# Kernel tuning notes

Measured on AMD Instinct MI355X. Metric: run time of the kernel, lower is better.

## Reference

```python
import jax, jax.numpy as jnp
import numpy as np

N_NODES = 50000
N_EDGES = 800000
D_IN = 64
D_HID = 64
D_OUT = 16


def setup_inputs() -> dict:
    key = jax.random.key(0)
    ks = jax.random.split(key, 20)
    features = jax.random.normal(ks[0], (N_NODES, D_IN), dtype=jnp.float32)
    src = jax.random.randint(ks[1], (N_EDGES,), 0, N_NODES)
    dst = jax.random.randint(ks[2], (N_EDGES,), 0, N_NODES)

    def lin(k, din, dout):
        bound = 1.0 / np.sqrt(din)
        k1, k2 = jax.random.split(k)
        W = jax.random.uniform(k1, (din, dout), jnp.float32, -bound, bound)
        b = jax.random.uniform(k2, (dout,), jnp.float32, -bound, bound)
        return W, b

    W0a, b0a = lin(ks[3], D_IN, D_HID)
    W0b, b0b = lin(ks[4], D_HID, D_HID)
    W1a, b1a = lin(ks[5], D_HID, D_HID)
    W1b, b1b = lin(ks[6], D_HID, D_HID)
    W2a, b2a = lin(ks[7], D_HID, D_HID)
    W2b, b2b = lin(ks[8], D_HID, D_HID)
    Wout, bout = lin(ks[9], D_HID, D_OUT)
    return {
        "features": features, "src": src, "dst": dst,
        "W0a": W0a, "b0a": b0a, "W0b": W0b, "b0b": b0b,
        "W1a": W1a, "b1a": b1a, "W1b": W1b, "b1b": b1b,
        "W2a": W2a, "b2a": b2a, "W2b": W2b, "b2b": b2b,
        "Wout": Wout, "bout": bout,
    }


def reference(features, src, dst,
              W0a, b0a, W0b, b0b,
              W1a, b1a, W1b, b1b,
              W2a, b2a, W2b, b2b,
              Wout, bout):
    N = features.shape[0]

    def gin_layer(h, Wa, ba, Wb, bb):
        # GINConv 'sum': gather source features along edges, scatter-sum to dst
        agg = jax.ops.segment_sum(h[src], dst, num_segments=N)  # [N, D]
        r = h + agg  # (1 + eps) * h + agg with eps = 0 (DGL default)
        # ApplyNodeFunc MLP: Linear -> ReLU -> Linear
        return jax.nn.relu(r @ Wa + ba) @ Wb + bb

    h = gin_layer(features, W0a, b0a, W0b, b0b)
    h = gin_layer(h, W1a, b1a, W1b, b1b)
    h = gin_layer(h, W2a, b2a, W2b, b2b)
    # dgl.mean_nodes over the single graph -> [1, D_HID]
    hg = jnp.mean(h, axis=0, keepdims=True)
    return hg @ Wout + bout  # [1, D_OUT]
```

## Files before the change

### kernel.cpp

```cpp
#include <hip/hip_runtime.h>
#include <hip/hip_bf16.h>


#define NNODES 50000
#define NEDGES 800000
#define DDIM   64
#define DOUT   16

#define CHUNK  4096
#define NB1    196
#define NBUCK  196
#define NB64   782
#define CVTB   1024

#define KCAP   1408

typedef unsigned int uint;
typedef unsigned short ushort;
typedef __attribute__((ext_vector_type(8))) short bf16x8;
typedef __attribute__((ext_vector_type(4))) float f32x4;
typedef __attribute__((ext_vector_type(2))) float f32x2;

#define LSTR 72

static __device__ __forceinline__ uint f2bf(float f) {
    uint u = __float_as_uint(f);
    return (u + 0x7fffu + ((u >> 16) & 1u)) >> 16;
}
static __device__ __forceinline__ float bf_lo(uint u) { return __uint_as_float(u << 16); }
static __device__ __forceinline__ float bf_hi(uint u) { return __uint_as_float(u & 0xffff0000u); }

#define ACC4(vv) do { f32x2 u_;                                   \
    u_.x = bf_lo((vv).x); u_.y = bf_hi((vv).x); c0 += u_;         \
    u_.x = bf_lo((vv).y); u_.y = bf_hi((vv).y); c1 += u_;         \
    u_.x = bf_lo((vv).z); u_.y = bf_hi((vv).z); c2 += u_;         \
    u_.x = bf_lo((vv).w); u_.y = bf_hi((vv).w); c3 += u_; } while (0)


__global__ __launch_bounds__(256) void s1_kernel(const int* __restrict__ src,
                                                 const int* __restrict__ dst,
                                                 uint* __restrict__ key,
                                                 int* __restrict__ gh,
                                                 const float2* __restrict__ fin,
                                                 uint* __restrict__ hb0,
                                                 uint* __restrict__ hb1,
                                                 const float* __restrict__ Wa0,
                                                 const float* __restrict__ Wb0,
                                                 const float* __restrict__ Wa1,
                                                 const float* __restrict__ Wb1,
                                                 const float* __restrict__ Wa2,
                                                 const float* __restrict__ Wb2,
                                                 uint* __restrict__ wWT,
                                                 float* __restrict__ part,
                                                 int* __restrict__ ticket) {
    __shared__ int h[NBUCK];
    int blk = blockIdx.x;
    int t = threadIdx.x;
    if (blk < NB1) {
        for (int i = t; i < NBUCK; i += 256) h[i] = 0;
        __syncthreads();
        int base = blk * CHUNK;
        int end = base + CHUNK < NEDGES ? base + CHUNK : NEDGES;
        for (int i = base + t; i < end; i += 256) {
            int d = dst[i];
            key[i] = ((uint)d << 16) | (uint)src[i];
            atomicAdd(&h[d >> 8], 1);
        }
        __syncthreads();
        for (int i = t; i < NBUCK; i += 256) gh[blk * NBUCK + i] = h[i];
        return;
    }
    int m = blk - NB1;
    if (m < CVTB) {
        for (int i = m * 256 + t; i < (NNODES + 1) * 32; i += CVTB * 256) {
            uint r = 0u;
            if (i < NNODES * 32) {
                float2 v = fin[i];
                r = f2bf(v.x) | (f2bf(v.y) << 16);
            }
            hb0[i] = r;
        }
        return;
    }
    m -= CVTB;
    if (m < 6) {
        const float* Wm = (m == 0) ? Wa0 : (m == 1) ? Wb0 : (m == 2) ? Wa1
                        : (m == 3) ? Wb1 : (m == 4) ? Wa2 : Wb2;
        for (int o = t; o < 2048; o += 256) {
            int nn = o >> 5, kk = o & 31;
            wWT[m * 2048 + o] = f2bf(Wm[(2 * kk) * 64 + nn]) |
                                (f2bf(Wm[(2 * kk + 1) * 64 + nn]) << 16);
        }
        return;
    }
    if (t < 64) part[t] = 0.f;
    if (t == 64) *ticket = 0;
    if (t >= 128 && t < 160) hb1[NNODES * 32 + (t - 128)] = 0u;
}


__global__ __launch_bounds__(256) void sort_offsets_a_kernel(const int* __restrict__ gh,
                                                             int* __restrict__ offraw,
                                                             int* __restrict__ tot) {
    __shared__ int s[256];
    int b = blockIdx.x;
    int i = threadIdx.x;
    int v = (i < NB1) ? gh[i * NBUCK + b] : 0;
    s[i] = v;
    __syncthreads();
    for (int off = 1; off < 256; off <<= 1) {
        int add = (i >= off) ? s[i - off] : 0;
        __syncthreads();
        s[i] += add;
        __syncthreads();
    }
    if (i < NB1) offraw[i * NBUCK + b] = s[i] - v;
    if (i == 255) tot[b] = s[255];
}


__global__ __launch_bounds__(256) void sort_scatter1_kernel(const uint* __restrict__ key,
                                                            const int* __restrict__ offraw,
                                                            const int* __restrict__ tot,
                                                            uint* __restrict__ out) {
    __shared__ int s[256];
    __shared__ int cur[NBUCK];
    int blk = blockIdx.x;
    int t = threadIdx.x;
    int v = (t < NBUCK) ? tot[t] : 0;
    s[t] = v;
    __syncthreads();
    for (int off = 1; off < 256; off <<= 1) {
        int add = (t >= off) ? s[t - off] : 0;
        __syncthreads();
        s[t] += add;
        __syncthreads();
    }
    if (t < NBUCK) cur[t] = (s[t] - v) + offraw[blk * NBUCK + t];
    __syncthreads();
    int base = blk * CHUNK;
    int end = base + CHUNK < NEDGES ? base + CHUNK : NEDGES;
    for (int j = base + t; j < end; j += 256) {
        uint k = key[j];
        int pos = atomicAdd(&cur[k >> 24], 1);
        out[pos] = k;
    }
}


__global__ __launch_bounds__(256) void sort_bucket_kernel(const uint* __restrict__ in,
                                                          const int* __restrict__ tot,
                                                          int* __restrict__ rowptr,
                                                          uint* __restrict__ out) {
    __shared__ int s[256];
    __shared__ int hh[256];
    __shared__ int cur[256];
    __shared__ int slo[2];
    int blk = blockIdx.x;
    int t = threadIdx.x;
    int v = (t < NBUCK) ? tot[t] : 0;
    s[t] = v;
    __syncthreads();
    for (int off = 1; off < 256; off <<= 1) {
        int add = (t >= off) ? s[t - off] : 0;
        __syncthreads();
        s[t] += add;
        __syncthreads();
    }
    if (t == blk) { slo[0] = s[t] - v; slo[1] = s[t]; }
    hh[t] = 0;
    __syncthreads();
    int lo = slo[0], hi = slo[1];
    for (int i = lo + t; i < hi; i += 256)
        atomicAdd(&hh[(in[i] >> 16) & 255], 1);
    __syncthreads();
    int hv = hh[t];
    s[t] = hv;
    __syncthreads();
    for (int off = 1; off < 256; off <<= 1) {
        int add = (t >= off) ? s[t - off] : 0;
        __syncthreads();
        s[t] += add;
        __syncthreads();
    }
    cur[t] = lo + s[t] - hv;
    __syncthreads();
    int node = (blk << 8) + t;
    if (node < NNODES) rowptr[node] = cur[t];
    if (blk == NBUCK - 1 && t == 0) rowptr[NNODES] = NEDGES;
    __syncthreads();
    for (int i = lo + t; i < hi; i += 256) {
        uint k = in[i];
        int pos = atomicAdd(&cur[(k >> 16) & 255], 1);
        out[pos] = k;
    }
}


__global__ __launch_bounds__(512, 4) void gin_layer_kernel(const uint4* __restrict__ h128,
                                                           const int* __restrict__ rowptr,
                                                           const uint* __restrict__ skey,
                                                           const uint4* __restrict__ wa4,
                                                           const uint4* __restrict__ wb4,
                                                           const float* __restrict__ ba,
                                                           const float* __restrict__ bb,
                                                           uint4* __restrict__ out128,
                                                           float* __restrict__ part,
                                                           int* __restrict__ ticket,
                                                           const float* __restrict__ Wout,
                                                           const float* __restrict__ bout,
                                                           float* __restrict__ out, int n) {
    __shared__ ushort sW1[64 * LSTR];
    __shared__ ushort sW2[64 * LSTR];
    __shared__ ushort sX[64 * LSTR];
    __shared__ float sba[64], sbb[64];
    __shared__ ushort sSrc[KCAP + 8];
    __shared__ int sRP[65];
    __shared__ float pool[256];
    __shared__ int lastFlag;

    int t = threadIdx.x;
    int node0 = blockIdx.x * 64;

    for (int i = t; i < 512; i += 512) {
        int nn = i >> 3, k8 = i & 7;
        *(uint4*)&sW1[nn * LSTR + k8 * 8] = wa4[nn * 8 + k8];
        *(uint4*)&sW2[nn * LSTR + k8 * 8] = wb4[nn * 8 + k8];
    }
    if (t < 64) { sba[t] = ba[t]; sbb[t] = bb[t]; }
    if (t >= 64 && t < 129) {
        int idx = node0 + (t - 64);
        sRP[t - 64] = rowptr[idx < n ? idx : n];
    }
    if (blockIdx.x == 0 && t >= 192 && t < 200) {
        uint4 z; z.x = 0; z.y = 0; z.z = 0; z.w = 0;
        out128[(size_t)NNODES * 8 + (t - 192)] = z;
    }
    int eBase = rowptr[node0];
    int vEnd = node0 + 64 < n ? node0 + 64 : n;
    int nE = rowptr[vEnd] - eBase;
    int nS = nE < KCAP ? nE : KCAP;
    for (int i = t; i < nS; i += 512) sSrc[i] = (ushort)skey[eBase + i];
    __syncthreads();

    int lane = t & 63;
    int w = t >> 6;
    int g = lane >> 3;
    uint p = (uint)(lane & 7);

    {
        int row = w * 8 + g;
        int v = node0 + row;
        if (v < n) {
            f32x2 c0 = {0.f, 0.f}, c1 = {0.f, 0.f}, c2 = {0.f, 0.f}, c3 = {0.f, 0.f};
            uint4 su = h128[(uint)v * 8u + p];
            ACC4(su);
            int e0r = sRP[row], e1r = sRP[row + 1];
            for (int e = e0r; e < e1r; e += 8) {
                int eo = e - eBase;
                uint k0 = sSrc[eo + 0];
                uint k1 = (e + 1 < e1r) ? (uint)sSrc[eo + 1] : 50000u;
                uint k2 = (e + 2 < e1r) ? (uint)sSrc[eo + 2] : 50000u;
                uint k3 = (e + 3 < e1r) ? (uint)sSrc[eo + 3] : 50000u;
                uint k4 = (e + 4 < e1r) ? (uint)sSrc[eo + 4] : 50000u;
                uint k5 = (e + 5 < e1r) ? (uint)sSrc[eo + 5] : 50000u;
                uint k6 = (e + 6 < e1r) ? (uint)sSrc[eo + 6] : 50000u;
                uint k7 = (e + 7 < e1r) ? (uint)sSrc[eo + 7] : 50000u;
                uint4 v0 = h128[k0 * 8u + p];
                uint4 v1 = h128[k1 * 8u + p];
                uint4 v2 = h128[k2 * 8u + p];
                uint4 v3 = h128[k3 * 8u + p];
                uint4 v4 = h128[k4 * 8u + p];
                uint4 v5 = h128[k5 * 8u + p];
                uint4 v6 = h128[k6 * 8u + p];
                uint4 v7 = h128[k7 * 8u + p];
                ACC4(v0); ACC4(v1); ACC4(v2); ACC4(v3);
                ACC4(v4); ACC4(v5); ACC4(v6); ACC4(v7);
            }
            uint4 o;
            o.x = f2bf(c0.x) | (f2bf(c0.y) << 16);
            o.y = f2bf(c1.x) | (f2bf(c1.y) << 16);
            o.z = f2bf(c2.x) | (f2bf(c2.y) << 16);
            o.w = f2bf(c3.x) | (f2bf(c3.y) << 16);
            *(uint4*)&sX[row * LSTR + (int)p * 8] = o;
        }
    }
    __syncthreads();

    int mc = lane & 15;
    int quad = lane >> 4;
    int m0 = w * 16;
    float csum[4] = {0.f, 0.f, 0.f, 0.f};

    if (w < 4) {
        bf16x8 xa0 = *(const bf16x8*)&sX[(m0 + mc) * LSTR + quad * 8];
        bf16x8 xa1 = *(const bf16x8*)&sX[(m0 + mc) * LSTR + 32 + quad * 8];
        ushort hreg[16];
#pragma unroll
        for (int c = 0; c < 4; c++) {
            bf16x8 b0 = *(const bf16x8*)&sW1[(c * 16 + mc) * LSTR + quad * 8];
            bf16x8 b1 = *(const bf16x8*)&sW1[(c * 16 + mc) * LSTR + 32 + quad * 8];
            f32x4 acc = {0.f, 0.f, 0.f, 0.f};
            acc = __builtin_amdgcn_mfma_f32_16x16x32_bf16(xa0, b0, acc, 0, 0, 0);
            acc = __builtin_amdgcn_mfma_f32_16x16x32_bf16(xa1, b1, acc, 0, 0, 0);
            int col = c * 16 + mc;
            float bias = sba[col];
#pragma unroll
            for (int r = 0; r < 4; r++)
                hreg[c * 4 + r] = (ushort)f2bf(fmaxf(acc[r] + bias, 0.f));
        }
#pragma unroll
        for (int c = 0; c < 4; c++) {
            int col = c * 16 + mc;
#pragma unroll
            for (int r = 0; r < 4; r++)
                sX[(m0 + quad * 4 + r) * LSTR + col] = hreg[c * 4 + r];
        }

        bool rok[4];
#pragma unroll
        for (int r = 0; r < 4; r++) rok[r] = (node0 + m0 + quad * 4 + r) < n;

        bf16x8 ha0 = *(const bf16x8*)&sX[(m0 + mc) * LSTR + quad * 8];
        bf16x8 ha1 = *(const bf16x8*)&sX[(m0 + mc) * LSTR + 32 + quad * 8];
#pragma unroll
        for (int c = 0; c < 4; c++) {
            bf16x8 b0 = *(const bf16x8*)&sW2[(c * 16 + mc) * LSTR + quad * 8];
            bf16x8 b1 = *(const bf16x8*)&sW2[(c * 16 + mc) * LSTR + 32 + quad * 8];
            f32x4 acc = {0.f, 0.f, 0.f, 0.f};
            acc = __builtin_amdgcn_mfma_f32_16x16x32_bf16(ha0, b0, acc, 0, 0, 0);
            acc = __builtin_amdgcn_mfma_f32_16x16x32_bf16(ha1, b1, acc, 0, 0, 0);
            int col = c * 16 + mc;
            float bias = sbb[col];
#pragma unroll
            for (int r = 0; r < 4; r++) {
                float val = acc[r] + bias;
                hreg[c * 4 + r] = (ushort)f2bf(val);
                csum[c] += rok[r] ? val : 0.f;
            }
        }
#pragma unroll
        for (int c = 0; c < 4; c++) {
            int col = c * 16 + mc;
#pragma unroll
            for (int r = 0; r < 4; r++)
                sX[(m0 + quad * 4 + r) * LSTR + col] = hreg[c * 4 + r];
        }

#pragma unroll
        for (int i = 0; i < 2; i++) {
            int idx = i * 64 + lane;
            int row16 = idx >> 3, q = idx & 7;
            int row = m0 + row16;
            int gr = node0 + row;
            if (gr < n) out128[(size_t)gr * 8 + q] = *(const uint4*)&sX[row * LSTR + q * 8];
        }
    }

    if (part) {
        if (w < 4) {
#pragma unroll
            for (int c = 0; c < 4; c++) {
                csum[c] += __shfl_xor(csum[c], 16);
                csum[c] += __shfl_xor(csum[c], 32);
            }
            if (quad == 0) {
#pragma unroll
                for (int c = 0; c < 4; c++) pool[w * 64 + c * 16 + mc] = csum[c];
            }
        }
        __syncthreads();
        if (t < 64) {
            float s4 = pool[t] + pool[64 + t] + pool[128 + t] + pool[192 + t];
            atomicAdd(&part[t], s4);
        }
        __syncthreads();
        if (t == 0) {
            __threadfence();
            int old = atomicAdd(ticket, 1);
            lastFlag = (old == NB64 - 1) ? 1 : 0;
        }
        __syncthreads();
        if (lastFlag) {
            if (t < 64)
                pool[t] = __hip_atomic_load(&part[t], __ATOMIC_RELAXED,
                                            __HIP_MEMORY_SCOPE_AGENT) * (1.0f / (float)NNODES);
            __syncthreads();
            if (t < DOUT) {
                float o = bout[t];
                for (int d = 0; d < DDIM; d++) o += pool[d] * Wout[d * DOUT + t];
                out[t] = o;
            }
        }
    }
}


extern "C" void kernel_launch(void* const* d_in, const int* in_sizes, int n_in,
                              void* d_out, int out_size, void* d_ws, size_t ws_size,
                              hipStream_t stream) {
    const float* features = (const float*)d_in[0];
    const int*   src      = (const int*)d_in[1];
    const int*   dst      = (const int*)d_in[2];
    const float* W0a = (const float*)d_in[3];  const float* b0a = (const float*)d_in[4];
    const float* W0b = (const float*)d_in[5];  const float* b0b = (const float*)d_in[6];
    const float* W1a = (const float*)d_in[7];  const float* b1a = (const float*)d_in[8];
    const float* W1b = (const float*)d_in[9];  const float* b1b = (const float*)d_in[10];
    const float* W2a = (const float*)d_in[11]; const float* b2a = (const float*)d_in[12];
    const float* W2b = (const float*)d_in[13]; const float* b2b = (const float*)d_in[14];
    const float* Wout = (const float*)d_in[15]; const float* bout = (const float*)d_in[16];
    float* out = (float*)d_out;

    int* gh     = (int*)d_ws;
    int* offraw = gh + 38416;
    int* tot    = offraw + 38416;
    int* rowptr = tot + 256;
    uint* keybuf = (uint*)(rowptr + 50016);
    uint* buf2   = keybuf + 800000;
    uint* hb0    = buf2 + 800000;
    uint* hb1    = hb0 + (NNODES + 1) * 32;
    float* part  = (float*)(hb1 + (NNODES + 1) * 32);
    int* ticket  = (int*)(part + 64);
    uint* wWT    = (uint*)(ticket + 4);

    s1_kernel<<<NB1 + CVTB + 7, 256, 0, stream>>>(src, dst, keybuf, gh,
                                                  (const float2*)features, hb0, hb1,
                                                  W0a, W0b, W1a, W1b, W2a, W2b,
                                                  wWT, part, ticket);
    sort_offsets_a_kernel<<<NBUCK, 256, 0, stream>>>(gh, offraw, tot);
    sort_scatter1_kernel<<<NB1, 256, 0, stream>>>(keybuf, offraw, tot, buf2);
    sort_bucket_kernel<<<NBUCK, 256, 0, stream>>>(buf2, tot, rowptr, keybuf);

    gin_layer_kernel<<<NB64, 512, 0, stream>>>((const uint4*)hb0, rowptr, keybuf,
                                               (const uint4*)(wWT + 0 * 2048),
                                               (const uint4*)(wWT + 1 * 2048),
                                               b0a, b0b, (uint4*)hb1,
                                               nullptr, nullptr, nullptr, nullptr, nullptr, NNODES);
    gin_layer_kernel<<<NB64, 512, 0, stream>>>((const uint4*)hb1, rowptr, keybuf,
                                               (const uint4*)(wWT + 2 * 2048),
                                               (const uint4*)(wWT + 3 * 2048),
                                               b1a, b1b, (uint4*)hb0,
                                               nullptr, nullptr, nullptr, nullptr, nullptr, NNODES);
    gin_layer_kernel<<<NB64, 512, 0, stream>>>((const uint4*)hb0, rowptr, keybuf,
                                               (const uint4*)(wWT + 4 * 2048),
                                               (const uint4*)(wWT + 5 * 2048),
                                               b2a, b2b, (uint4*)hb1,
                                               part, ticket, Wout, bout, out, NNODES);
}
```

Measured before the change: 202.2 us.

## Gather neighbor features from an FP8 copy and skip the final layer's store

Adds a parallel FP8 (e4m3) copy of the node features, written alongside the bf16 copy in the conversion kernel and in each layer's epilogue. The edge gather now reads 8-byte FP8 rows instead of 16-byte bf16 rows, halving gather traffic, and the inner loop is unrolled to 16 edges. The self term still uses bf16. The last layer skips writing node features because only the pooled sum is needed. The cost is precision: FP8 neighbor values may exceed the accuracy tolerance, and each layer does extra conversion work and writes.

```diff
diff --git a/kernel.cpp b/kernel.cpp
--- a/kernel.cpp
+++ b/kernel.cpp
@@ -36,14 +36,22 @@
     u_.x = bf_lo((vv).z); u_.y = bf_hi((vv).z); c2 += u_;         \
     u_.x = bf_lo((vv).w); u_.y = bf_hi((vv).w); c3 += u_; } while (0)
 
+#define ACCP(wv) do {                                                     \
+    c0 += __builtin_amdgcn_cvt_pk_f32_fp8((int)(wv).x, false);            \
+    c1 += __builtin_amdgcn_cvt_pk_f32_fp8((int)(wv).x, true);             \
+    c2 += __builtin_amdgcn_cvt_pk_f32_fp8((int)(wv).y, false);            \
+    c3 += __builtin_amdgcn_cvt_pk_f32_fp8((int)(wv).y, true);             \
+} while (0)
+
 
 __global__ __launch_bounds__(256) void s1_kernel(const int* __restrict__ src,
                                                  const int* __restrict__ dst,
                                                  uint* __restrict__ key,
                                                  int* __restrict__ gh,
-                                                 const float2* __restrict__ fin,
-                                                 uint* __restrict__ hb0,
-                                                 uint* __restrict__ hb1,
+                                                 const float4* __restrict__ fin4,
+                                                 uint2* __restrict__ hb0_2,
+                                                 uint* __restrict__ p0u,
+                                                 uint* __restrict__ p1u,
                                                  const float* __restrict__ Wa0,
                                                  const float* __restrict__ Wb0,
                                                  const float* __restrict__ Wa1,
@@ -72,13 +80,18 @@
     }
     int m = blk - NB1;
     if (m < CVTB) {
-        for (int i = m * 256 + t; i < (NNODES + 1) * 32; i += CVTB * 256) {
-            uint r = 0u;
-            if (i < NNODES * 32) {
-                float2 v = fin[i];
-                r = f2bf(v.x) | (f2bf(v.y) << 16);
-            }
-            hb0[i] = r;
+        for (int i = m * 256 + t; i < (NNODES + 1) * 16; i += CVTB * 256) {
+            uint2 hb; uint pk = 0u;
+            if (i < NNODES * 16) {
+                float4 v = fin4[i];
+                hb.x = f2bf(v.x) | (f2bf(v.y) << 16);
+                hb.y = f2bf(v.z) | (f2bf(v.w) << 16);
+                int w0 = __builtin_amdgcn_cvt_pk_fp8_f32(v.x, v.y, 0, false);
+                w0 = __builtin_amdgcn_cvt_pk_fp8_f32(v.z, v.w, w0, true);
+                pk = (uint)w0;
+            } else { hb.x = 0u; hb.y = 0u; }
+            hb0_2[i] = hb;
+            p0u[i] = pk;
         }
         return;
     }
@@ -95,7 +108,7 @@
     }
     if (t < 64) part[t] = 0.f;
     if (t == 64) *ticket = 0;
-    if (t >= 128 && t < 160) hb1[NNODES * 32 + (t - 128)] = 0u;
+    if (t >= 128 && t < 144) p1u[NNODES * 16 + (t - 128)] = 0u;
 }
 
 
@@ -198,6 +211,7 @@
 
 
 __global__ __launch_bounds__(512, 4) void gin_layer_kernel(const uint4* __restrict__ h128,
+                                                           const uint2* __restrict__ pin,
                                                            const int* __restrict__ rowptr,
                                                            const uint* __restrict__ skey,
                                                            const uint4* __restrict__ wa4,
@@ -205,6 +219,7 @@
                                                            const float* __restrict__ ba,
                                                            const float* __restrict__ bb,
                                                            uint4* __restrict__ out128,
+                                                           uint2* __restrict__ pout,
                                                            float* __restrict__ part,
                                                            int* __restrict__ ticket,
                                                            const float* __restrict__ Wout,
@@ -214,7 +229,7 @@
     __shared__ ushort sW2[64 * LSTR];
     __shared__ ushort sX[64 * LSTR];
     __shared__ float sba[64], sbb[64];
-    __shared__ ushort sSrc[KCAP + 8];
+    __shared__ ushort sSrc[KCAP + 16];
     __shared__ int sRP[65];
     __shared__ float pool[256];
     __shared__ int lastFlag;
@@ -231,10 +246,6 @@
     if (t >= 64 && t < 129) {
         int idx = node0 + (t - 64);
         sRP[t - 64] = rowptr[idx < n ? idx : n];
-    }
-    if (blockIdx.x == 0 && t >= 192 && t < 200) {
-        uint4 z; z.x = 0; z.y = 0; z.z = 0; z.w = 0;
-        out128[(size_t)NNODES * 8 + (t - 192)] = z;
     }
     int eBase = rowptr[node0];
     int vEnd = node0 + 64 < n ? node0 + 64 : n;
@@ -256,26 +267,44 @@
             uint4 su = h128[(uint)v * 8u + p];
             ACC4(su);
             int e0r = sRP[row], e1r = sRP[row + 1];
-            for (int e = e0r; e < e1r; e += 8) {
+            for (int e = e0r; e < e1r; e += 16) {
                 int eo = e - eBase;
                 uint k0 = sSrc[eo + 0];
-                uint k1 = (e + 1 < e1r) ? (uint)sSrc[eo + 1] : 50000u;
-                uint k2 = (e + 2 < e1r) ? (uint)sSrc[eo + 2] : 50000u;
-                uint k3 = (e + 3 < e1r) ? (uint)sSrc[eo + 3] : 50000u;
-                uint k4 = (e + 4 < e1r) ? (uint)sSrc[eo + 4] : 50000u;
-                uint k5 = (e + 5 < e1r) ? (uint)sSrc[eo + 5] : 50000u;
-                uint k6 = (e + 6 < e1r) ? (uint)sSrc[eo + 6] : 50000u;
-                uint k7 = (e + 7 < e1r) ? (uint)sSrc[eo + 7] : 50000u;
-                uint4 v0 = h128[k0 * 8u + p];
-                uint4 v1 = h128[k1 * 8u + p];
-                uint4 v2 = h128[k2 * 8u + p];
-                uint4 v3 = h128[k3 * 8u + p];
-                uint4 v4 = h128[k4 * 8u + p];
-                uint4 v5 = h128[k5 * 8u + p];
-                uint4 v6 = h128[k6 * 8u + p];
-                uint4 v7 = h128[k7 * 8u + p];
-                ACC4(v0); ACC4(v1); ACC4(v2); ACC4(v3);
-                ACC4(v4); ACC4(v5); ACC4(v6); ACC4(v7);
+                uint k1  = (e + 1  < e1r) ? (uint)sSrc[eo + 1]  : 50000u;
+                uint k2  = (e + 2  < e1r) ? (uint)sSrc[eo + 2]  : 50000u;
+                uint k3  = (e + 3  < e1r) ? (uint)sSrc[eo + 3]  : 50000u;
+                uint k4  = (e + 4  < e1r) ? (uint)sSrc[eo + 4]  : 50000u;
+                uint k5  = (e + 5  < e1r) ? (uint)sSrc[eo + 5]  : 50000u;
+                uint k6  = (e + 6  < e1r) ? (uint)sSrc[eo + 6]  : 50000u;
+                uint k7  = (e + 7  < e1r) ? (uint)sSrc[eo + 7]  : 50000u;
+                uint k8  = (e + 8  < e1r) ? (uint)sSrc[eo + 8]  : 50000u;
+                uint k9  = (e + 9  < e1r) ? (uint)sSrc[eo + 9]  : 50000u;
+                uint k10 = (e + 10 < e1r) ? (uint)sSrc[eo + 10] : 50000u;
+                uint k11 = (e + 11 < e1r) ? (uint)sSrc[eo + 11] : 50000u;
+                uint k12 = (e + 12 < e1r) ? (uint)sSrc[eo + 12] : 50000u;
+                uint k13 = (e + 13 < e1r) ? (uint)sSrc[eo + 13] : 50000u;
+                uint k14 = (e + 14 < e1r) ? (uint)sSrc[eo + 14] : 50000u;
+                uint k15 = (e + 15 < e1r) ? (uint)sSrc[eo + 15] : 50000u;
+                uint2 v0  = pin[k0  * 8u + p];
+                uint2 v1  = pin[k1  * 8u + p];
+                uint2 v2  = pin[k2  * 8u + p];
+                uint2 v3  = pin[k3  * 8u + p];
+                uint2 v4  = pin[k4  * 8u + p];
+                uint2 v5  = pin[k5  * 8u + p];
+                uint2 v6  = pin[k6  * 8u + p];
+                uint2 v7  = pin[k7  * 8u + p];
+                uint2 v8  = pin[k8  * 8u + p];
+                uint2 v9  = pin[k9  * 8u + p];
+                uint2 v10 = pin[k10 * 8u + p];
+                uint2 v11 = pin[k11 * 8u + p];
+                uint2 v12 = pin[k12 * 8u + p];
+                uint2 v13 = pin[k13 * 8u + p];
+                uint2 v14 = pin[k14 * 8u + p];
+                uint2 v15 = pin[k15 * 8u + p];
+                ACCP(v0); ACCP(v1); ACCP(v2); ACCP(v3);
+                ACCP(v4); ACCP(v5); ACCP(v6); ACCP(v7);
+                ACCP(v8); ACCP(v9); ACCP(v10); ACCP(v11);
+                ACCP(v12); ACCP(v13); ACCP(v14); ACCP(v15);
             }
             uint4 o;
             o.x = f2bf(c0.x) | (f2bf(c0.y) << 16);
@@ -339,21 +368,36 @@
                 csum[c] += rok[r] ? val : 0.f;
             }
         }
-#pragma unroll
-        for (int c = 0; c < 4; c++) {
-            int col = c * 16 + mc;
-#pragma unroll
-            for (int r = 0; r < 4; r++)
-                sX[(m0 + quad * 4 + r) * LSTR + col] = hreg[c * 4 + r];
-        }
-
-#pragma unroll
-        for (int i = 0; i < 2; i++) {
-            int idx = i * 64 + lane;
-            int row16 = idx >> 3, q = idx & 7;
-            int row = m0 + row16;
-            int gr = node0 + row;
-            if (gr < n) out128[(size_t)gr * 8 + q] = *(const uint4*)&sX[row * LSTR + q * 8];
+
+        if (out128) {
+#pragma unroll
+            for (int c = 0; c < 4; c++) {
+                int col = c * 16 + mc;
+#pragma unroll
+                for (int r = 0; r < 4; r++)
+                    sX[(m0 + quad * 4 + r) * LSTR + col] = hreg[c * 4 + r];
+            }
+#pragma unroll
+            for (int i = 0; i < 2; i++) {
+                int idx = i * 64 + lane;
+                int row16 = idx >> 3, q = idx & 7;
+                int row = m0 + row16;
+                int gr = node0 + row;
+                if (gr < n) {
+                    uint4 o = *(const uint4*)&sX[row * LSTR + q * 8];
+                    out128[(size_t)gr * 8 + q] = o;
+                    float f0 = bf_lo(o.x), f1 = bf_hi(o.x);
+                    float f2 = bf_lo(o.y), f3 = bf_hi(o.y);
+                    float f4 = bf_lo(o.z), f5 = bf_hi(o.z);
+                    float f6 = bf_lo(o.w), f7 = bf_hi(o.w);
+                    int w0 = __builtin_amdgcn_cvt_pk_fp8_f32(f0, f1, 0, false);
+                    w0 = __builtin_amdgcn_cvt_pk_fp8_f32(f2, f3, w0, true);
+                    int w1 = __builtin_amdgcn_cvt_pk_fp8_f32(f4, f5, 0, false);
+                    w1 = __builtin_amdgcn_cvt_pk_fp8_f32(f6, f7, w1, true);
+                    uint2 pk; pk.x = (uint)w0; pk.y = (uint)w1;
+                    pout[(size_t)gr * 8 + q] = pk;
+                }
+            }
         }
     }
 
@@ -419,31 +463,37 @@
     uint* buf2   = keybuf + 800000;
     uint* hb0    = buf2 + 800000;
     uint* hb1    = hb0 + (NNODES + 1) * 32;
-    float* part  = (float*)(hb1 + (NNODES + 1) * 32);
+    uint* p0u    = hb1 + (NNODES + 1) * 32;
+    uint* p1u    = p0u + (NNODES + 1) * 16;
+    float* part  = (float*)(p1u + (NNODES + 1) * 16);
     int* ticket  = (int*)(part + 64);
     uint* wWT    = (uint*)(ticket + 4);
 
     s1_kernel<<<NB1 + CVTB + 7, 256, 0, stream>>>(src, dst, keybuf, gh,
-                                                  (const float2*)features, hb0, hb1,
+                                                  (const float4*)features,
+                                                  (uint2*)hb0, p0u, p1u,
                                                   W0a, W0b, W1a, W1b, W2a, W2b,
                                                   wWT, part, ticket);
     sort_offsets_a_kernel<<<NBUCK, 256, 0, stream>>>(gh, offraw, tot);
     sort_scatter1_kernel<<<NB1, 256, 0, stream>>>(keybuf, offraw, tot, buf2);
     sort_bucket_kernel<<<NBUCK, 256, 0, stream>>>(buf2, tot, rowptr, keybuf);
 
-    gin_layer_kernel<<<NB64, 512, 0, stream>>>((const uint4*)hb0, rowptr, keybuf,
+    gin_layer_kernel<<<NB64, 512, 0, stream>>>((const uint4*)hb0, (const uint2*)p0u,
+                                               rowptr, keybuf,
                                                (const uint4*)(wWT + 0 * 2048),
                                                (const uint4*)(wWT + 1 * 2048),
-                                               b0a, b0b, (uint4*)hb1,
+                                               b0a, b0b, (uint4*)hb1, (uint2*)p1u,
                                                nullptr, nullptr, nullptr, nullptr, nullptr, NNODES);
-    gin_layer_kernel<<<NB64, 512, 0, stream>>>((const uint4*)hb1, rowptr, keybuf,
+    gin_layer_kernel<<<NB64, 512, 0, stream>>>((const uint4*)hb1, (const uint2*)p1u,
+                                               rowptr, keybuf,
                                                (const uint4*)(wWT + 2 * 2048),
                                                (const uint4*)(wWT + 3 * 2048),
-                                               b1a, b1b, (uint4*)hb0,
+                                               b1a, b1b, (uint4*)hb0, (uint2*)p0u,
                                                nullptr, nullptr, nullptr, nullptr, nullptr, NNODES);
-    gin_layer_kernel<<<NB64, 512, 0, stream>>>((const uint4*)hb0, rowptr, keybuf,
+    gin_layer_kernel<<<NB64, 512, 0, stream>>>((const uint4*)hb0, (const uint2*)p0u,
+                                               rowptr, keybuf,
                                                (const uint4*)(wWT + 4 * 2048),
                                                (const uint4*)(wWT + 5 * 2048),
-                                               b2a, b2b, (uint4*)hb1,
+                                               b2a, b2b, nullptr, nullptr,
                                                part, ticket, Wout, bout, out, NNODES);
 }
```

Result: faster. 191.5 us (-5.3%).
